# Optimization experiments

Measured on AMD Instinct MI355X. Metric: run time of the kernel, lower is better.

## Reference

```python
import jax, jax.numpy as jnp
import numpy as np

N_EMBD = 768
N_HEADS = 12
HEAD_DIM = N_EMBD // N_HEADS
B, T = 2, 4096


def setup_inputs() -> dict:
    key = jax.random.key(0)
    k1, k2, k3 = jax.random.split(key, 3)
    x = jax.random.normal(k1, (B, T, N_EMBD), dtype=jnp.float32)
    # torch Linear(in, out) weight has shape (out, in); x @ W.T == x @ W_j with W_j = W.T
    w_qkv = jax.random.normal(k2, (N_EMBD, 3 * N_EMBD), dtype=jnp.float32) * (1.0 / np.sqrt(N_EMBD))
    w_proj = jax.random.normal(k3, (N_EMBD, N_EMBD), dtype=jnp.float32) * (1.0 / np.sqrt(N_EMBD))
    return {"x": x, "w_qkv": w_qkv, "w_proj": w_proj}


def reference(x, w_qkv, w_proj):
    Bx, Tx, C = x.shape
    qkv = x @ w_qkv                                  # [B,T,3C]
    q, k, v = jnp.split(qkv, 3, axis=2)
    def to_heads(t):
        return t.reshape(Bx, Tx, N_HEADS, HEAD_DIM).transpose(0, 2, 1, 3)  # [B,H,T,D]
    q, k, v = to_heads(q), to_heads(k), to_heads(v)
    scale = HEAD_DIM ** -0.5
    att = jnp.einsum('bhqd,bhkd->bhqk', q, k) * scale  # [B,H,T,T]
    causal = jnp.tril(jnp.ones((Tx, Tx), dtype=bool))
    att = jnp.where(causal[None, None], att, -jnp.inf)
    att = jax.nn.softmax(att, axis=-1)
    y = jnp.einsum('bhqk,bhkd->bhqd', att, v)          # [B,H,T,D]
    y = y.transpose(0, 2, 1, 3).reshape(Bx, Tx, C)
    return y @ w_proj
```

## Files before the change

### kernel.cpp

```cpp
#include <hip/hip_runtime.h>
#include <hip/hip_bf16.h>

#define Bn 2
#define Tn 4096
#define Cn 768
#define Hn 12
#define Dn 64
#define Mn (Bn * Tn)
#define PAD 72

typedef __attribute__((ext_vector_type(8))) short bf16x8;
typedef __attribute__((ext_vector_type(4))) short bf16x4;
typedef __attribute__((ext_vector_type(4))) float f32x4;

typedef const __attribute__((address_space(1))) unsigned int* gas_ptr;
typedef __attribute__((address_space(3))) unsigned int* las_ptr;

__device__ __forceinline__ float b2f(unsigned short u) {
    return __uint_as_float(((unsigned int)u) << 16);
}
__device__ __forceinline__ unsigned short f2b(float f) {
    unsigned int x = __float_as_uint(f);
    x += 0x7FFFu + ((x >> 16) & 1u);
    return (unsigned short)(x >> 16);
}
__device__ __forceinline__ unsigned int cvt_pk_bf16(float lo, float hi) {
    unsigned int r;
    asm("v_cvt_pk_bf16_f32 %0, %1, %2" : "=v"(r) : "v"(lo), "v"(hi));
    return r;
}

__device__ __forceinline__ void async_ld16(const unsigned short* g, unsigned short* l) {
    __builtin_amdgcn_global_load_lds((gas_ptr)(const void*)g, (las_ptr)(void*)l, 16, 0, 0);
}

__global__ __launch_bounds__(256) void prep1_k(
    const void* __restrict__ wqkv, unsigned short* __restrict__ wqkvT,
    const void* __restrict__ x, unsigned short* __restrict__ xb,
    const void* __restrict__ wproj, unsigned short* __restrict__ wprojT,
    int* __restrict__ flag)
{
    __shared__ unsigned short Ts[64][PAD];
    __shared__ int anyf;
    const int tid = threadIdx.x;
    if (tid == 0) anyf = 0;
    __syncthreads();
    {
        int4 v = reinterpret_cast<const int4*>(wqkv)[tid];
        const unsigned short* u = reinterpret_cast<const unsigned short*>(&v);
        int bad = 0;
#pragma unroll
        for (int j = 0; j < 8; ++j) {
            const unsigned int e = (u[j] >> 7) & 0xFFu;
            bad |= (e >= 0x88u) ? 1 : 0;
        }
        if (bad) atomicOr(&anyf, 1);
    }
    __syncthreads();
    const bool f32 = (anyf != 0);
    if (tid == 0 && blockIdx.x == 0) *flag = anyf;

    if (blockIdx.x >= 432 && blockIdx.x < 3504) {
        const size_t i = ((size_t)(blockIdx.x - 432) * 256 + tid) * 8;
        union { int4 v; unsigned short u[8]; } pk;
        if (f32) {
            const float* p = (const float*)x + i;
            float4 a = *reinterpret_cast<const float4*>(p);
            float4 b = *reinterpret_cast<const float4*>(p + 4);
            float t[8] = {a.x, a.y, a.z, a.w, b.x, b.y, b.z, b.w};
#pragma unroll
            for (int j = 0; j < 8; ++j) pk.u[j] = f2b(t[j]);
        } else {
            pk.v = *reinterpret_cast<const int4*>((const unsigned short*)x + i);
        }
        *reinterpret_cast<int4*>(xb + i) = pk.v;
        return;
    }

    const bool isW2 = (blockIdx.x >= 3504);
    const void* in = isW2 ? wproj : wqkv;
    unsigned short* out = isW2 ? wprojT : wqkvT;
    const int K = Cn;
    const int N = isW2 ? Cn : 3 * Cn;
    const int id = isW2 ? ((int)blockIdx.x - 3504) : (int)blockIdx.x;
    const int ncols = N / 64;
    const int nB = (id % ncols) * 64, kB = (id / ncols) * 64;
#pragma unroll
    for (int it = 0; it < 2; ++it) {
        const int r = (tid >> 3) + it * 32;
        const int c = (tid & 7) * 8;
        float t[8];
        if (f32) {
            const float* p = (const float*)in + (size_t)(kB + r) * N + nB + c;
            float4 a = *reinterpret_cast<const float4*>(p);
            float4 b = *reinterpret_cast<const float4*>(p + 4);
            t[0]=a.x;t[1]=a.y;t[2]=a.z;t[3]=a.w;t[4]=b.x;t[5]=b.y;t[6]=b.z;t[7]=b.w;
        } else {
            int4 v = *reinterpret_cast<const int4*>((const unsigned short*)in + (size_t)(kB + r) * N + nB + c);
            const unsigned short* u = reinterpret_cast<const unsigned short*>(&v);
#pragma unroll
            for (int j = 0; j < 8; ++j) t[j] = b2f(u[j]);
        }
#pragma unroll
        for (int j = 0; j < 8; ++j) Ts[c + j][r] = f2b(t[j]);
    }
    __syncthreads();
#pragma unroll
    for (int it = 0; it < 2; ++it) {
        const int n = (tid >> 3) + it * 32;
        const int k = (tid & 7) * 8;
        *reinterpret_cast<int4*>(out + (size_t)(nB + n) * K + kB + k) =
            *reinterpret_cast<const int4*>(&Ts[n][k]);
    }
}

__global__ __launch_bounds__(256) void transpose_w_k(
    const void* __restrict__ in, unsigned short* __restrict__ out,
    int K, int N, const int* __restrict__ flag)
{
    __shared__ unsigned short Ts[64][PAD];
    const int tid = threadIdx.x;
    const int kB = blockIdx.y * 64, nB = blockIdx.x * 64;
    const bool f32 = (*flag != 0);
#pragma unroll
    for (int it = 0; it < 2; ++it) {
        const int r = (tid >> 3) + it * 32;
        const int c = (tid & 7) * 8;
        float t[8];
        if (f32) {
            const float* p = (const float*)in + (size_t)(kB + r) * N + nB + c;
            float4 a = *reinterpret_cast<const float4*>(p);
            float4 b = *reinterpret_cast<const float4*>(p + 4);
            t[0]=a.x;t[1]=a.y;t[2]=a.z;t[3]=a.w;t[4]=b.x;t[5]=b.y;t[6]=b.z;t[7]=b.w;
        } else {
            int4 v = *reinterpret_cast<const int4*>((const unsigned short*)in + (size_t)(kB + r) * N + nB + c);
            const unsigned short* u = reinterpret_cast<const unsigned short*>(&v);
#pragma unroll
            for (int j = 0; j < 8; ++j) t[j] = b2f(u[j]);
        }
#pragma unroll
        for (int j = 0; j < 8; ++j) Ts[c + j][r] = f2b(t[j]);
    }
    __syncthreads();
#pragma unroll
    for (int it = 0; it < 2; ++it) {
        const int n = (tid >> 3) + it * 32;
        const int k = (tid & 7) * 8;
        *reinterpret_cast<int4*>(out + (size_t)(nB + n) * K + kB + k) =
            *reinterpret_cast<const int4*>(&Ts[n][k]);
    }
}

template <int EPI>
__global__ __launch_bounds__(256) void gemm_lds(
    const unsigned short* __restrict__ A, const unsigned short* __restrict__ Bt,
    void* __restrict__ Out, unsigned short* __restrict__ Qo,
    unsigned short* __restrict__ Ko, unsigned short* __restrict__ Vo,
    int M, int N, int K, const int* __restrict__ flag)
{
    __shared__ unsigned short As[8192];
    __shared__ unsigned short Bs[8192];
    const int tid = threadIdx.x;
    const int w = tid >> 6, l = tid & 63;
    const int l15 = l & 15, l4 = l >> 4;

    const int gx = (int)gridDim.x;
    const int nwg = gx * (int)gridDim.y;
    int fid = (int)blockIdx.y * gx + (int)blockIdx.x;
    if ((nwg & 7) == 0) fid = (fid & 7) * (nwg >> 3) + (fid >> 3);
    const int rowBase = (fid / gx) * 128;
    const int colBase = (fid % gx) * 128;

    const int mq = (w & 1) * 64, nq = (w >> 1) * 64;
    const bool f32 = (*flag != 0);

    const int laneRow = l15, laneK = l4 * 8;

    f32x4 acc[4][4];
#pragma unroll
    for (int i = 0; i < 4; ++i)
#pragma unroll
        for (int j = 0; j < 4; ++j) acc[i][j] = (f32x4){0.f, 0.f, 0.f, 0.f};

    for (int k0 = 0; k0 < K; k0 += 64) {
        __syncthreads();
#pragma unroll
        for (int j = 0; j < 4; ++j) {
            const int c = w * 4 + j;
            const int mt_g = c >> 1, kh = c & 1;
            const size_t ga = (size_t)(rowBase + mt_g * 16 + laneRow) * K + k0 + kh * 32 + laneK;
            const size_t gb = (size_t)(colBase + mt_g * 16 + laneRow) * K + k0 + kh * 32 + laneK;
            async_ld16(A + ga, &As[c * 512]);
            async_ld16(Bt + gb, &Bs[c * 512]);
        }
        __syncthreads();

#pragma unroll
        for (int kh = 0; kh < 2; ++kh) {
            bf16x8 af[4], bf[4];
#pragma unroll
            for (int mt = 0; mt < 4; ++mt)
                af[mt] = *reinterpret_cast<const bf16x8*>(
                    &As[(((mq >> 4) + mt) * 2 + kh) * 512 + l * 8]);
#pragma unroll
            for (int nt = 0; nt < 4; ++nt)
                bf[nt] = *reinterpret_cast<const bf16x8*>(
                    &Bs[(((nq >> 4) + nt) * 2 + kh) * 512 + l * 8]);
#pragma unroll
            for (int mt = 0; mt < 4; ++mt)
#pragma unroll
                for (int nt = 0; nt < 4; ++nt)
                    acc[mt][nt] = __builtin_amdgcn_mfma_f32_16x16x32_bf16(af[mt], bf[nt], acc[mt][nt], 0, 0, 0);
        }
    }

#pragma unroll
    for (int mt = 0; mt < 4; ++mt)
#pragma unroll
        for (int nt = 0; nt < 4; ++nt) {
            const int n0 = colBase + nq + nt * 16 + l15;
            const int m0 = rowBase + mq + mt * 16 + l4 * 4;
            if (EPI == 0) {
#pragma unroll
                for (int i = 0; i < 4; ++i) {
                    if (f32) ((float*)Out)[(size_t)(m0 + i) * N + n0] = acc[mt][nt][i];
                    else ((unsigned short*)Out)[(size_t)(m0 + i) * N + n0] = f2b(acc[mt][nt][i]);
                }
            } else {
                const int sec = n0 / 768;
                const int cc = n0 - sec * 768;
                const int h = cc >> 6, d = cc & 63;
                const int b = m0 >> 12, t0 = m0 & 4095;
                if (sec < 2) {
                    unsigned short* dst = (sec == 0) ? Qo : Ko;
#pragma unroll
                    for (int i = 0; i < 4; ++i)
                        dst[(((size_t)(b * Hn + h) * Tn + t0 + i) * Dn) + d] = f2b(acc[mt][nt][i]);
                } else {
                    union { unsigned int u[2]; uint2 v; } pk;
                    pk.u[0] = (unsigned int)f2b(acc[mt][nt][0]) |
                              ((unsigned int)f2b(acc[mt][nt][1]) << 16);
                    pk.u[1] = (unsigned int)f2b(acc[mt][nt][2]) |
                              ((unsigned int)f2b(acc[mt][nt][3]) << 16);
                    *reinterpret_cast<uint2*>(
                        &Vo[(((size_t)(b * Hn + h) * Dn + d) * Tn) + t0]) = pk.v;
                }
            }
        }
}

__global__ __launch_bounds__(256) void gemm_qkv_fb(
    const void* __restrict__ A, const unsigned short* __restrict__ Bt,
    unsigned short* __restrict__ Qo, unsigned short* __restrict__ Ko,
    unsigned short* __restrict__ Vo, int M, int N, int K,
    const int* __restrict__ flag)
{
    __shared__ unsigned short As[128 * PAD];
    __shared__ unsigned short Bs[128 * PAD];
    const int tid = threadIdx.x;
    const int w = tid >> 6, l = tid & 63;
    const int l15 = l & 15, l4 = l >> 4;
    const int rowBase = blockIdx.y * 128;
    const int colBase = blockIdx.x * 128;
    const int mq = (w & 1) * 64, nq = (w >> 1) * 64;
    const bool af32 = (*flag != 0);

    f32x4 acc[4][4];
#pragma unroll
    for (int i = 0; i < 4; ++i)
#pragma unroll
        for (int j = 0; j < 4; ++j) acc[i][j] = (f32x4){0.f, 0.f, 0.f, 0.f};

    for (int k0 = 0; k0 < K; k0 += 64) {
        __syncthreads();
#pragma unroll
        for (int it = 0; it < 4; ++it) {
            const int s = tid + it * 256;
            const int r = s >> 3, c = (s & 7) * 8;
            union { int4 v; unsigned short u[8]; } pk;
            if (af32) {
                const float* p = (const float*)A + (size_t)(rowBase + r) * K + k0 + c;
                float4 a = *reinterpret_cast<const float4*>(p);
                float4 b = *reinterpret_cast<const float4*>(p + 4);
                float t[8] = {a.x, a.y, a.z, a.w, b.x, b.y, b.z, b.w};
#pragma unroll
                for (int j = 0; j < 8; ++j) pk.u[j] = f2b(t[j]);
            } else {
                pk.v = *reinterpret_cast<const int4*>(
                    (const unsigned short*)A + (size_t)(rowBase + r) * K + k0 + c);
            }
            *reinterpret_cast<int4*>(&As[r * PAD + c]) = pk.v;
            *reinterpret_cast<int4*>(&Bs[r * PAD + c]) =
                *reinterpret_cast<const int4*>(Bt + (size_t)(colBase + r) * K + k0 + c);
        }
        __syncthreads();
#pragma unroll
        for (int kk = 0; kk < 64; kk += 32) {
            bf16x8 af[4], bf[4];
#pragma unroll
            for (int mt = 0; mt < 4; ++mt)
                af[mt] = *reinterpret_cast<const bf16x8*>(&As[(mq + mt * 16 + l15) * PAD + kk + l4 * 8]);
#pragma unroll
            for (int nt = 0; nt < 4; ++nt)
                bf[nt] = *reinterpret_cast<const bf16x8*>(&Bs[(nq + nt * 16 + l15) * PAD + kk + l4 * 8]);
#pragma unroll
            for (int mt = 0; mt < 4; ++mt)
#pragma unroll
                for (int nt = 0; nt < 4; ++nt)
                    acc[mt][nt] = __builtin_amdgcn_mfma_f32_16x16x32_bf16(af[mt], bf[nt], acc[mt][nt], 0, 0, 0);
        }
    }

#pragma unroll
    for (int mt = 0; mt < 4; ++mt)
#pragma unroll
        for (int i = 0; i < 4; ++i) {
            const int m = rowBase + mq + mt * 16 + l4 * 4 + i;
#pragma unroll
            for (int nt = 0; nt < 4; ++nt) {
                const int n0 = colBase + nq + nt * 16 + l15;
                const int sec = n0 / 768;
                const int cc = n0 - sec * 768;
                const int h = cc >> 6, d = cc & 63;
                const int b = m >> 12, t = m & 4095;
                unsigned short* dst = (sec == 0) ? Qo : (sec == 1) ? Ko : Vo;
                dst[(((size_t)(b * Hn + h) * Tn + t) * Dn) + d] = f2b(acc[mt][nt][i]);
            }
        }
}

__global__ __launch_bounds__(256, 4) void attn_mfma2(
    const unsigned short* __restrict__ Q, const unsigned short* __restrict__ K,
    const unsigned short* __restrict__ Vt, unsigned short* __restrict__ Y)
{
    __shared__ unsigned short Ks[2][8 * 512];
    __shared__ unsigned short Vs[2][8 * 512];

    const int tid = threadIdx.x;
    const int w = tid >> 6, l = tid & 63;
    const int l15 = l & 15, l4 = l >> 4;

    const int f = (int)blockIdx.y * 32 + (int)blockIdx.x;
    const int r8 = f & 7, j = f >> 3;
    const int bh = r8 * 3 + (j >> 5);
    const int xq = j & 31;

    const size_t base = (size_t)bh * Tn * Dn;
    const float sc = 0.125f * 1.44269504088896f;
    const int b = bh / Hn, h = bh - b * Hn;

    const int vlb = (l4 >> 1) * 256 + l15 * 16 + (l4 & 1) * 8;

    for (int half = 0; half < 2; ++half) {
        const int t = half ? xq : (63 - xq);
        const int q0 = t * 64;
        const int qrow = q0 + w * 16 + l15;

        bf16x8 aq[2];
#pragma unroll
        for (int kh = 0; kh < 2; ++kh)
            aq[kh] = *reinterpret_cast<const bf16x8*>(
                Q + base + (size_t)qrow * Dn + kh * 32 + l4 * 8);

        f32x4 o[4];
#pragma unroll
        for (int dt = 0; dt < 4; ++dt) o[dt] = (f32x4){0.f, 0.f, 0.f, 0.f};
        float lsum = 0.f;

        const int nst = (q0 >> 6) + 1;

        __syncthreads();
#pragma unroll
        for (int jj = 0; jj < 2; ++jj) {
            const int c = w * 2 + jj;
            const int sub = c >> 1, kh = c & 1;
            async_ld16(K + base + (size_t)(sub * 16 + l15) * Dn + kh * 32 + l4 * 8,
                       &Ks[0][c * 512]);
            async_ld16(Vt + base + (size_t)(sub * 16 + l15) * Tn + kh * 32 + l4 * 8,
                       &Vs[0][c * 512]);
        }

        int cur = 0;
        for (int s = 0; s < nst; ++s) {
            const int k0 = s << 6;
            __syncthreads();

            if (s + 1 < nst) {
                const int kn = k0 + 64;
#pragma unroll
                for (int jj = 0; jj < 2; ++jj) {
                    const int c = w * 2 + jj;
                    const int sub = c >> 1, kh = c & 1;
                    async_ld16(K + base + (size_t)(kn + sub * 16 + l15) * Dn + kh * 32 + l4 * 8,
                               &Ks[cur ^ 1][c * 512]);
                    async_ld16(Vt + base + (size_t)(sub * 16 + l15) * Tn + kn + kh * 32 + l4 * 8,
                               &Vs[cur ^ 1][c * 512]);
                }
            }

            f32x4 sfr[4];
            __builtin_amdgcn_s_setprio(1);
#pragma unroll
            for (int tt = 0; tt < 4; ++tt) {
                bf16x8 ak0 = *reinterpret_cast<const bf16x8*>(&Ks[cur][(tt * 2 + 0) * 512 + l * 8]);
                bf16x8 ak1 = *reinterpret_cast<const bf16x8*>(&Ks[cur][(tt * 2 + 1) * 512 + l * 8]);
                f32x4 z = (f32x4){0.f, 0.f, 0.f, 0.f};
                z = __builtin_amdgcn_mfma_f32_16x16x32_bf16(ak0, aq[0], z, 0, 0, 0);
                z = __builtin_amdgcn_mfma_f32_16x16x32_bf16(ak1, aq[1], z, 0, 0, 0);
                sfr[tt] = z;
            }
            __builtin_amdgcn_s_setprio(0);

            const bool need_mask = (k0 + 63 > q0);
            float p[4][4];
#pragma unroll
            for (int tt = 0; tt < 4; ++tt)
#pragma unroll
                for (int i = 0; i < 4; ++i) {
                    float s2 = sfr[tt][i] * sc;
                    if (need_mask && (k0 + tt * 16 + l4 * 4 + i > qrow)) s2 = -1e30f;
                    const float e = __builtin_amdgcn_exp2f(s2);
                    p[tt][i] = e;
                    lsum += e;
                }

            bf16x4 pa[4];
#pragma unroll
            for (int tt = 0; tt < 4; ++tt) {
                union { unsigned int u[2]; bf16x4 v; } uu;
                uu.u[0] = cvt_pk_bf16(p[tt][0], p[tt][1]);
                uu.u[1] = cvt_pk_bf16(p[tt][2], p[tt][3]);
                pa[tt] = uu.v;
            }

            const char* vb = (const char*)&Vs[cur][0];
            __builtin_amdgcn_s_setprio(1);
#pragma unroll
            for (int dt = 0; dt < 4; ++dt) {
#pragma unroll
                for (int tt = 0; tt < 4; ++tt) {
                    bf16x4 bv = *reinterpret_cast<const bf16x4*>(vb + dt * 2048 + tt * 512 + vlb);
                    o[dt] = __builtin_amdgcn_mfma_f32_16x16x16bf16_1k(pa[tt], bv, o[dt], 0, 0, 0);
                }
            }
            __builtin_amdgcn_s_setprio(0);
            cur ^= 1;
        }

        lsum += __shfl_xor(lsum, 16);
        lsum += __shfl_xor(lsum, 32);

#pragma unroll
        for (int i = 0; i < 4; ++i) {
            const float lv = __shfl(lsum, (l & 48) + (l4 * 4 + i));
            const float inv = 1.0f / lv;
            const int row = q0 + w * 16 + l4 * 4 + i;
#pragma unroll
            for (int dt = 0; dt < 4; ++dt)
                Y[((size_t)(b * Tn + row)) * Cn + h * 64 + dt * 16 + l15] = f2b(o[dt][i] * inv);
        }
    }
}

__global__ __launch_bounds__(256, 3) void attn_mfma_fb(
    const unsigned short* __restrict__ Q, const unsigned short* __restrict__ K,
    const unsigned short* __restrict__ V, unsigned short* __restrict__ Y)
{
    __shared__ unsigned short Ks[96 * PAD];
    __shared__ unsigned short Vtl[96 * PAD];
    __shared__ unsigned short Ps[96 * PAD];

    const int tid = threadIdx.x;
    const int w = tid >> 6, l = tid & 63;
    const int l15 = l & 15, l4 = l >> 4;
    const int bh = blockIdx.y;
    const size_t base = (size_t)bh * Tn * Dn;
    const float sc = 0.125f * 1.44269504088896f;
    const int b = bh / Hn, h = bh - b * Hn;

    for (int half = 0; half < 2; ++half) {
        const int t = half ? (int)blockIdx.x : (63 - (int)blockIdx.x);
        const int q0 = t * 64;

        bf16x8 aq[2];
#pragma unroll
        for (int kh = 0; kh < 2; ++kh)
            aq[kh] = *reinterpret_cast<const bf16x8*>(
                Q + base + (size_t)(q0 + w * 16 + l15) * Dn + kh * 32 + l4 * 8);

        f32x4 o[4];
#pragma unroll
        for (int dt = 0; dt < 4; ++dt) o[dt] = (f32x4){0.f, 0.f, 0.f, 0.f};
        float l_i[4] = {0.f, 0.f, 0.f, 0.f};

        const int kend = q0 + 64;
        for (int k0 = 0; k0 < kend; k0 += 64) {
            __syncthreads();
#pragma unroll
            for (int it = 0; it < 2; ++it) {
                const int s = tid + it * 256;
                const int r = s >> 3, c = (s & 7) * 8;
                *reinterpret_cast<int4*>(&Ks[r * PAD + c]) =
                    *reinterpret_cast<const int4*>(K + base + (size_t)(k0 + r) * Dn + c);
            }
#pragma unroll
            for (int it = 0; it < 2; ++it) {
                const int r = tid & 63, d0 = (tid >> 6) * 8 + it * 32;
                int4 vv = *reinterpret_cast<const int4*>(V + base + (size_t)(k0 + r) * Dn + d0);
                const unsigned short* vu = reinterpret_cast<const unsigned short*>(&vv);
#pragma unroll
                for (int j = 0; j < 8; ++j) Vtl[(d0 + j) * PAD + r] = vu[j];
            }
            __syncthreads();

            f32x4 sfr[4];
#pragma unroll
            for (int tt = 0; tt < 4; ++tt) {
                bf16x8 bk0 = *reinterpret_cast<const bf16x8*>(&Ks[(tt * 16 + l15) * PAD + l4 * 8]);
                bf16x8 bk1 = *reinterpret_cast<const bf16x8*>(&Ks[(tt * 16 + l15) * PAD + 32 + l4 * 8]);
                f32x4 z = (f32x4){0.f, 0.f, 0.f, 0.f};
                z = __builtin_amdgcn_mfma_f32_16x16x32_bf16(aq[0], bk0, z, 0, 0, 0);
                z = __builtin_amdgcn_mfma_f32_16x16x32_bf16(aq[1], bk1, z, 0, 0, 0);
                sfr[tt] = z;
            }

            const bool need_mask = (k0 + 63 > q0);
            float p[4][4];
#pragma unroll
            for (int tt = 0; tt < 4; ++tt) {
                const int cb = k0 + tt * 16 + l15;
                const int rb = q0 + w * 16 + l4 * 4;
#pragma unroll
                for (int i = 0; i < 4; ++i) {
                    float s = sfr[tt][i] * sc;
                    if (need_mask && (cb > rb + i)) s = -1e30f;
                    const float e = exp2f(s);
                    p[tt][i] = e;
                    l_i[i] += e;
                }
            }

#pragma unroll
            for (int tt = 0; tt < 4; ++tt)
#pragma unroll
                for (int i = 0; i < 4; ++i)
                    Ps[(w * 16 + l4 * 4 + i) * PAD + tt * 16 + l15] = f2b(p[tt][i]);

            bf16x8 ap0 = *reinterpret_cast<const bf16x8*>(&Ps[(w * 16 + l15) * PAD + l4 * 8]);
            bf16x8 ap1 = *reinterpret_cast<const bf16x8*>(&Ps[(w * 16 + l15) * PAD + 32 + l4 * 8]);
#pragma unroll
            for (int dt = 0; dt < 4; ++dt) {
                bf16x8 bv0 = *reinterpret_cast<const bf16x8*>(&Vtl[(dt * 16 + l15) * PAD + l4 * 8]);
                bf16x8 bv1 = *reinterpret_cast<const bf16x8*>(&Vtl[(dt * 16 + l15) * PAD + 32 + l4 * 8]);
                o[dt] = __builtin_amdgcn_mfma_f32_16x16x32_bf16(ap0, bv0, o[dt], 0, 0, 0);
                o[dt] = __builtin_amdgcn_mfma_f32_16x16x32_bf16(ap1, bv1, o[dt], 0, 0, 0);
            }
        }

#pragma unroll
        for (int i = 0; i < 4; ++i)
#pragma unroll
            for (int off = 1; off < 16; off <<= 1) l_i[i] += __shfl_xor(l_i[i], off);

#pragma unroll
        for (int i = 0; i < 4; ++i) {
            const float inv = 1.0f / l_i[i];
            const int row = q0 + w * 16 + l4 * 4 + i;
#pragma unroll
            for (int dt = 0; dt < 4; ++dt)
                Y[((size_t)(b * Tn + row)) * Cn + h * 64 + dt * 16 + l15] = f2b(o[dt][i] * inv);
        }
    }
}

extern "C" void kernel_launch(void* const* d_in, const int* in_sizes, int n_in,
                              void* d_out, int out_size, void* d_ws, size_t ws_size,
                              hipStream_t stream)
{
    const void* x = d_in[0];
    const void* wqkv = d_in[1];
    const void* wproj = d_in[2];
    const size_t HSZ = (size_t)Bn * Hn * Tn * Dn;
    unsigned short* q = (unsigned short*)d_ws;
    unsigned short* k = q + HSZ;
    unsigned short* v = k + HSZ;
    unsigned short* R = v + HSZ;
    unsigned short* wqkvT = R;
    unsigned short* y = R;
    unsigned short* wprojT = q;
    const bool big = ws_size >= (size_t)5 * HSZ * 2 + 16;
    unsigned short* xb = R + HSZ;
    int* flag = big ? (int*)(xb + HSZ) : (int*)(R + HSZ);
    unsigned short* wprojT2 = xb + HSZ + 64;
    const bool big2 = big &&
        ws_size >= ((size_t)5 * HSZ + 64 + (size_t)Cn * Cn) * 2 + 16;

    if (big) {
        prep1_k<<<big2 ? 3648 : 3504, 256, 0, stream>>>(
            wqkv, wqkvT, x, xb, wproj, big2 ? wprojT2 : xb, flag);
        gemm_lds<1><<<dim3(3 * Cn / 128, Mn / 128), 256, 0, stream>>>(
            xb, wqkvT, nullptr, q, k, v, Mn, 3 * Cn, Cn, flag);
        attn_mfma2<<<dim3(Tn / 128, Bn * Hn), 256, 0, stream>>>(q, k, v, y);
        if (big2) {
            gemm_lds<0><<<dim3(Cn / 128, Mn / 128), 256, 0, stream>>>(
                y, wprojT2, d_out, nullptr, nullptr, nullptr, Mn, Cn, Cn, flag);
        } else {
            transpose_w_k<<<dim3(Cn / 64, Cn / 64), 256, 0, stream>>>(wproj, wprojT, Cn, Cn, flag);
            gemm_lds<0><<<dim3(Cn / 128, Mn / 128), 256, 0, stream>>>(
                y, wprojT, d_out, nullptr, nullptr, nullptr, Mn, Cn, Cn, flag);
        }
    } else {
        prep1_k<<<432, 256, 0, stream>>>(wqkv, wqkvT, x, (unsigned short*)d_ws,
                                         wproj, (unsigned short*)d_ws, flag);
        gemm_qkv_fb<<<dim3(3 * Cn / 128, Mn / 128), 256, 0, stream>>>(
            x, wqkvT, q, k, v, Mn, 3 * Cn, Cn, flag);
        attn_mfma_fb<<<dim3(Tn / 128, Bn * Hn), 256, 0, stream>>>(q, k, v, y);
        transpose_w_k<<<dim3(Cn / 64, Cn / 64), 256, 0, stream>>>(wproj, wprojT, Cn, Cn, flag);
        gemm_lds<0><<<dim3(Cn / 128, Mn / 128), 256, 0, stream>>>(
            y, wprojT, d_out, nullptr, nullptr, nullptr, Mn, Cn, Cn, flag);
    }
}
```

Measured before the change: 287.5 us.

## Double-buffer LDS tiles in GEMM to overlap global loads with MFMA

The GEMM K-loop now uses two LDS buffers with a 32-wide K step. It issues the async global-to-LDS loads for the next tile before computing on the current one, and drops one of the two barriers per iteration. The goal is to hide global memory latency behind the matrix-core work. In exchange there are twice as many loop iterations, and correctness depends on the async loads being complete before the next barrier.

```diff
diff --git a/kernel.cpp b/kernel.cpp
--- a/kernel.cpp
+++ b/kernel.cpp
@@ -158,8 +158,8 @@
     unsigned short* __restrict__ Ko, unsigned short* __restrict__ Vo,
     int M, int N, int K, const int* __restrict__ flag)
 {
-    __shared__ unsigned short As[8192];
-    __shared__ unsigned short Bs[8192];
+    __shared__ unsigned short As[2][8 * 512];
+    __shared__ unsigned short Bs[2][8 * 512];
     const int tid = threadIdx.x;
     const int w = tid >> 6, l = tid & 63;
     const int l15 = l & 15, l4 = l >> 4;
@@ -174,44 +174,51 @@
     const int mq = (w & 1) * 64, nq = (w >> 1) * 64;
     const bool f32 = (*flag != 0);
 
-    const int laneRow = l15, laneK = l4 * 8;
-
     f32x4 acc[4][4];
 #pragma unroll
     for (int i = 0; i < 4; ++i)
 #pragma unroll
         for (int j = 0; j < 4; ++j) acc[i][j] = (f32x4){0.f, 0.f, 0.f, 0.f};
 
-    for (int k0 = 0; k0 < K; k0 += 64) {
+#pragma unroll
+    for (int jj = 0; jj < 2; ++jj) {
+        const int c = w * 2 + jj;
+        async_ld16(A + (size_t)(rowBase + c * 16 + l15) * K + l4 * 8, &As[0][c * 512]);
+        async_ld16(Bt + (size_t)(colBase + c * 16 + l15) * K + l4 * 8, &Bs[0][c * 512]);
+    }
+
+    const int nk = K >> 5;
+    int cur = 0;
+    for (int s = 0; s < nk; ++s) {
         __syncthreads();
-#pragma unroll
-        for (int j = 0; j < 4; ++j) {
-            const int c = w * 4 + j;
-            const int mt_g = c >> 1, kh = c & 1;
-            const size_t ga = (size_t)(rowBase + mt_g * 16 + laneRow) * K + k0 + kh * 32 + laneK;
-            const size_t gb = (size_t)(colBase + mt_g * 16 + laneRow) * K + k0 + kh * 32 + laneK;
-            async_ld16(A + ga, &As[c * 512]);
-            async_ld16(Bt + gb, &Bs[c * 512]);
-        }
-        __syncthreads();
-
-#pragma unroll
-        for (int kh = 0; kh < 2; ++kh) {
-            bf16x8 af[4], bf[4];
-#pragma unroll
-            for (int mt = 0; mt < 4; ++mt)
-                af[mt] = *reinterpret_cast<const bf16x8*>(
-                    &As[(((mq >> 4) + mt) * 2 + kh) * 512 + l * 8]);
+
+        if (s + 1 < nk) {
+            const int kn = (s + 1) << 5;
+#pragma unroll
+            for (int jj = 0; jj < 2; ++jj) {
+                const int c = w * 2 + jj;
+                async_ld16(A + (size_t)(rowBase + c * 16 + l15) * K + kn + l4 * 8,
+                           &As[cur ^ 1][c * 512]);
+                async_ld16(Bt + (size_t)(colBase + c * 16 + l15) * K + kn + l4 * 8,
+                           &Bs[cur ^ 1][c * 512]);
+            }
+        }
+
+        bf16x8 af[4], bf[4];
+#pragma unroll
+        for (int mt = 0; mt < 4; ++mt)
+            af[mt] = *reinterpret_cast<const bf16x8*>(
+                &As[cur][((mq >> 4) + mt) * 512 + l * 8]);
+#pragma unroll
+        for (int nt = 0; nt < 4; ++nt)
+            bf[nt] = *reinterpret_cast<const bf16x8*>(
+                &Bs[cur][((nq >> 4) + nt) * 512 + l * 8]);
+#pragma unroll
+        for (int mt = 0; mt < 4; ++mt)
 #pragma unroll
             for (int nt = 0; nt < 4; ++nt)
-                bf[nt] = *reinterpret_cast<const bf16x8*>(
-                    &Bs[(((nq >> 4) + nt) * 2 + kh) * 512 + l * 8]);
-#pragma unroll
-            for (int mt = 0; mt < 4; ++mt)
-#pragma unroll
-                for (int nt = 0; nt < 4; ++nt)
-                    acc[mt][nt] = __builtin_amdgcn_mfma_f32_16x16x32_bf16(af[mt], bf[nt], acc[mt][nt], 0, 0, 0);
-        }
+                acc[mt][nt] = __builtin_amdgcn_mfma_f32_16x16x32_bf16(af[mt], bf[nt], acc[mt][nt], 0, 0, 0);
+        cur ^= 1;
     }
 
 #pragma unroll
```

Measured after the change: 277.9 us. -3.3%, faster.
